# Optimization experiments

Measured on AMD Instinct MI355X. Metric: run time of the kernel, lower is better.

## Reference

```python
import jax, jax.numpy as jnp
import numpy as np

EPS = 1e-5
NUM_HEADS = 4


def _layer_norm(x, g, b):
    m = jnp.mean(x, axis=-1, keepdims=True)
    v = jnp.mean((x - m) ** 2, axis=-1, keepdims=True)
    return (x - m) / jnp.sqrt(v + EPS) * g + b


def setup_inputs() -> dict:
    key = jax.random.key(0)
    ks = jax.random.split(key, 32)
    B, N, ND, TD, L = 100000, 20, 128, 64, 2
    HD = 128  # num_heads * attention_dim
    CD = ND + TD  # 192
    s = 0.02
    inp = {
        "node_features": jax.random.normal(ks[0], (B, ND), jnp.float32),
        "neighbor_features": jax.random.normal(ks[1], (B, N, ND), jnp.float32),
        "node_times": jax.random.uniform(ks[2], (B,), jnp.float32),
        "neighbor_times": jax.random.uniform(ks[3], (B, N), jnp.float32),
        "time_freq": jax.random.normal(ks[4], (TD,), jnp.float32),
        "time_phase": jnp.zeros((TD,), jnp.float32),
        "Wq": jax.random.normal(ks[5], (L, CD, HD), jnp.float32) * s,
        "bq": jnp.zeros((L, HD), jnp.float32),
        "Wk": jax.random.normal(ks[6], (L, CD, HD), jnp.float32) * s,
        "bk": jnp.zeros((L, HD), jnp.float32),
        "Wv": jax.random.normal(ks[7], (L, CD, HD), jnp.float32) * s,
        "bv": jnp.zeros((L, HD), jnp.float32),
        "Wo": jax.random.normal(ks[8], (L, HD, ND), jnp.float32) * s,
        "bo": jnp.zeros((L, ND), jnp.float32),
        "W1": jax.random.normal(ks[9], (L, ND, 2 * ND), jnp.float32) * s,
        "b1": jnp.zeros((L, 2 * ND), jnp.float32),
        "W2": jax.random.normal(ks[10], (L, 2 * ND, ND), jnp.float32) * s,
        "b2": jnp.zeros((L, ND), jnp.float32),
        "g1": jnp.ones((L, ND), jnp.float32),
        "be1": jnp.zeros((L, ND), jnp.float32),
        "g2": jnp.ones((L, ND), jnp.float32),
        "be2": jnp.zeros((L, ND), jnp.float32),
        "Wc1": jax.random.normal(ks[11], (ND, ND // 2), jnp.float32) * s,
        "bc1": jnp.zeros((ND // 2,), jnp.float32),
        "Wc2": jax.random.normal(ks[12], (ND // 2, 1), jnp.float32) * s,
        "bc2": jnp.zeros((1,), jnp.float32),
        "mask": jax.random.randint(ks[13], (B, N), 0, 2, jnp.int32),
    }
    return inp


def reference(node_features, neighbor_features, node_times, neighbor_times,
              time_freq, time_phase, Wq, bq, Wk, bk, Wv, bv, Wo, bo,
              W1, b1, W2, b2, g1, be1, g2, be2, Wc1, bc1, Wc2, bc2, mask):
    L, _, HD = Wq.shape
    B, N, ND = neighbor_features.shape
    H = NUM_HEADS
    D = HD // H
    scale = 1.0 / np.sqrt(D).astype(np.float32)
    # time encodings (Bochner): cos(t * w + phi)
    tq = jnp.cos(node_times[:, None] * time_freq + time_phase)          # [B, TD]
    tk = jnp.cos(neighbor_times[..., None] * time_freq + time_phase)   # [B, N, TD]
    kcomb = jnp.concatenate([neighbor_features, tk], axis=-1)           # [B, N, CD]
    pad = (mask == 0)[:, None, :]                                       # [B, 1, N]
    x = node_features
    for l in range(L):
        qcomb = jnp.concatenate([x, tq], axis=-1)                       # [B, CD]
        q = (qcomb @ Wq[l] + bq[l]).reshape(B, H, D)
        k = (kcomb @ Wk[l] + bk[l]).reshape(B, N, H, D)
        v = (kcomb @ Wv[l] + bv[l]).reshape(B, N, H, D)
        scores = jnp.einsum('bhd,bnhd->bhn', q, k) * scale              # [B, H, N]
        scores = jnp.where(pad, jnp.float32(-1e9), scores)
        w = jax.nn.softmax(scores, axis=-1)
        a = jnp.einsum('bhn,bnhd->bhd', w, v).reshape(B, HD)
        attn = a @ Wo[l] + bo[l]                                        # [B, ND]
        x = _layer_norm(x + attn, g1[l], be1[l])
        ff = jax.nn.relu(x @ W1[l] + b1[l]) @ W2[l] + b2[l]
        x = _layer_norm(x + ff, g2[l], be2[l])
    h = jax.nn.relu(x @ Wc1 + bc1)
    return jax.nn.sigmoid(h @ Wc2 + bc2)                                # [B, 1]
```

## Files before the change

kernel.cpp:

```cpp
#include <hip/hip_runtime.h>

#define BB 100000
#define NN 20
#define ND 128
#define TD 64
#define CD 192
#define HD 128
#define NH 4
#define DH 32
#define NL 2

typedef __attribute__((ext_vector_type(8))) short bf16x8;
typedef __attribute__((ext_vector_type(4))) float f32x4;

static __device__ __forceinline__ float bf2f(unsigned short u) {
  return __uint_as_float(((unsigned)u) << 16);
}
static __device__ __forceinline__ unsigned short f2bf(float x) {
  unsigned b = __float_as_uint(x);
  return (unsigned short)((b + 0x7FFFu + ((b >> 16) & 1u)) >> 16);
}
static __device__ __forceinline__ bf16x8 load_a8(const float* p) {
  float4 a = *(const float4*)p, b = *(const float4*)(p + 4);
  bf16x8 r;
  r[0] = (short)f2bf(a.x); r[1] = (short)f2bf(a.y);
  r[2] = (short)f2bf(a.z); r[3] = (short)f2bf(a.w);
  r[4] = (short)f2bf(b.x); r[5] = (short)f2bf(b.y);
  r[6] = (short)f2bf(b.z); r[7] = (short)f2bf(b.w);
  return r;
}


__global__ __launch_bounds__(256) void conv_w(
    const float* __restrict__ Wq, const float* __restrict__ Wk,
    const float* __restrict__ Wv, const float* __restrict__ Wo,
    const float* __restrict__ W1, const float* __restrict__ W2,
    unsigned short* __restrict__ WF) {
  int t = blockIdx.x;
  int l = t / 304, tt = t % 304;
#pragma unroll
  for (int e = 0; e < 2; ++e) {
    int idx = threadIdx.x * 2 + e;
    int lane = idx >> 3, j = idx & 7;
    int wk = ((lane >> 4) << 3) + j;
    int c16 = lane & 15;
    float v;
    if (tt < 48) {
      int kt = tt >> 3, n2 = tt & 7;
      v = Wq[((size_t)l * CD + kt * 32 + wk) * HD + n2 * 16 + c16];
    } else if (tt < 96) {
      int t2 = tt - 48; int h = t2 / 12, n2 = t2 % 12;
      v = Wk[((size_t)l * CD + n2 * 16 + c16) * HD + h * 32 + wk];
    } else if (tt < 144) {
      int t2 = tt - 96; int h = t2 / 12, r2 = t2 % 12, kt = r2 >> 1, n2 = r2 & 1;
      v = Wv[((size_t)l * CD + kt * 32 + wk) * HD + h * 32 + n2 * 16 + c16];
    } else if (tt < 176) {
      int t2 = tt - 144; int kt = t2 >> 3, n2 = t2 & 7;
      v = Wo[((size_t)l * HD + kt * 32 + wk) * ND + n2 * 16 + c16];
    } else if (tt < 240) {
      int t2 = tt - 176; int kt = t2 >> 4, n2 = t2 & 15;
      v = W1[((size_t)l * ND + kt * 32 + wk) * (2 * ND) + n2 * 16 + c16];
    } else {
      int t2 = tt - 240; int kt = t2 >> 3, n2 = t2 & 7;
      v = W2[((size_t)l * 2 * ND + kt * 32 + wk) * ND + n2 * 16 + c16];
    }
    WF[(size_t)l * 155648 + (size_t)tt * 512 + idx] = f2bf(v);
  }
}

__global__ __launch_bounds__(256) void prep_tq(
    const float* __restrict__ ntime, const float* __restrict__ tf,
    const float* __restrict__ tp, float* __restrict__ tqf) {
  int i = blockIdx.x * 256 + threadIdx.x;
  int b = i >> 6, j = i & 63;
  tqf[i] = __cosf(ntime[b] * tf[j] + tp[j]);
}

__global__ __launch_bounds__(256) void prep_mb(const int* __restrict__ mask,
                                               unsigned* __restrict__ mb) {
  int e = blockIdx.x * 256 + threadIdx.x;
  if (e < BB) {
    unsigned m = 0;
    for (int n = 0; n < NN; ++n)
      m |= (mask[(size_t)e * NN + n] != 0 ? 1u : 0u) << n;
    mb[e] = m;
  }
}

template <int TN, int ABF, int OBF>
__global__ __launch_bounds__(256) void gemm16(
    const void* __restrict__ A, int lda,
    const float* __restrict__ A2, int lda2, int ksplit,
    const unsigned short* __restrict__ BF,
    int ktiles, int ntiles, int aKoffMul, int cColMul, int segBMul,
    const float* __restrict__ bias,
    void* __restrict__ C, int ldc, int relu) {
  const int tid = threadIdx.x;
  const int wv = tid >> 6, lane = tid & 63;
  const int NW = blockDim.x >> 6;
  const int m0 = blockIdx.x << 4;
  const int seg = blockIdx.y;
  const int arow = m0 + (lane & 15);
  const int kgrp = (lane >> 4) << 3;
  const int aK = seg * aKoffMul;
  const unsigned short* Bseg = BF + (size_t)seg * segBMul * 512;
  f32x4 acc[TN];
#pragma unroll
  for (int i = 0; i < TN; ++i) acc[i] = f32x4{0.f, 0.f, 0.f, 0.f};
  for (int kt = 0; kt < ktiles; ++kt) {
    bf16x8 af;
    if (kt * 32 >= ksplit) {
      af = load_a8(A2 + (size_t)arow * lda2 + (kt * 32 - ksplit) + kgrp);
    } else if (ABF) {
      af = *(const bf16x8*)((const unsigned short*)A + (size_t)arow * lda + aK +
                            kt * 32 + kgrp);
    } else {
      af = load_a8((const float*)A + (size_t)arow * lda + aK + kt * 32 + kgrp);
    }
#pragma unroll
    for (int i = 0; i < TN; ++i) {
      int nt = wv + NW * i;
      bf16x8 bf = *(const bf16x8*)(Bseg + (((size_t)(kt * ntiles + nt)) << 9) +
                                   (lane << 3));
      acc[i] = __builtin_amdgcn_mfma_f32_16x16x32_bf16(af, bf, acc[i], 0, 0, 0);
    }
  }
  const int crow = m0 + ((lane >> 4) << 2);
#pragma unroll
  for (int i = 0; i < TN; ++i) {
    int nt = wv + NW * i;
    int col = seg * cColMul + nt * 16 + (lane & 15);
    float bv = bias ? bias[col] : 0.f;
#pragma unroll
    for (int rr = 0; rr < 4; ++rr) {
      float v = acc[i][rr] + bv;
      if (relu) v = fmaxf(v, 0.f);
      if (OBF)
        ((unsigned short*)C)[(size_t)(crow + rr) * ldc + col] = f2bf(v);
      else
        ((float*)C)[(size_t)(crow + rr) * ldc + col] = v;
    }
  }
}

template <int ABF, int CLS>
__global__ __launch_bounds__(256) void gemm_ln(
    const void* __restrict__ A, int lda, int ktiles,
    const unsigned short* __restrict__ BF,
    const float* __restrict__ bias, const float* __restrict__ res,
    const float* __restrict__ gamma, const float* __restrict__ beta,
    float* __restrict__ xout,
    const float* __restrict__ Wc1, const float* __restrict__ bc1,
    const float* __restrict__ Wc2, const float* __restrict__ bc2,
    float* __restrict__ out) {
  __shared__ float Cs[16][132];
  __shared__ float hsh[CLS ? 16 : 1][64];
  const int tid = threadIdx.x;
  const int wv = tid >> 6, lane = tid & 63;
  const int m0 = blockIdx.x << 4;
  const int arow = m0 + (lane & 15);
  const int kgrp = (lane >> 4) << 3;
  const int nt0 = wv, nt1 = wv + 4;
  f32x4 acc0 = {0.f, 0.f, 0.f, 0.f}, acc1 = {0.f, 0.f, 0.f, 0.f};
  for (int kt = 0; kt < ktiles; ++kt) {
    bf16x8 af;
    if (ABF)
      af = *(const bf16x8*)((const unsigned short*)A + (size_t)arow * lda +
                            kt * 32 + kgrp);
    else
      af = load_a8((const float*)A + (size_t)arow * lda + kt * 32 + kgrp);
    bf16x8 b0 = *(const bf16x8*)(BF + (((size_t)(kt * 8 + nt0)) << 9) + (lane << 3));
    bf16x8 b1 = *(const bf16x8*)(BF + (((size_t)(kt * 8 + nt1)) << 9) + (lane << 3));
    acc0 = __builtin_amdgcn_mfma_f32_16x16x32_bf16(af, b0, acc0, 0, 0, 0);
    acc1 = __builtin_amdgcn_mfma_f32_16x16x32_bf16(af, b1, acc1, 0, 0, 0);
  }
  {
    const int lrow = (lane >> 4) << 2;
    int c0 = nt0 * 16 + (lane & 15), c1 = nt1 * 16 + (lane & 15);
    float bv0 = bias[c0], bv1 = bias[c1];
#pragma unroll
    for (int rr = 0; rr < 4; ++rr) {
      Cs[lrow + rr][c0] = acc0[rr] + bv0;
      Cs[lrow + rr][c1] = acc1[rr] + bv1;
    }
  }
  __syncthreads();
#pragma unroll
  for (int rr = 0; rr < 4; ++rr) {
    int rw = wv * 4 + rr;
    size_t grow = (size_t)(m0 + rw) * ND;
    float y0 = Cs[rw][lane] + res[grow + lane];
    float y1 = Cs[rw][lane + 64] + res[grow + lane + 64];
    float s = y0 + y1, ss = y0 * y0 + y1 * y1;
#pragma unroll
    for (int off = 32; off > 0; off >>= 1) {
      s += __shfl_xor(s, off);
      ss += __shfl_xor(ss, off);
    }
    float mean = s * (1.f / ND);
    float var = ss * (1.f / ND) - mean * mean;
    float rstd = rsqrtf(var + 1e-5f);
    float x0 = (y0 - mean) * rstd * gamma[lane] + beta[lane];
    float x1 = (y1 - mean) * rstd * gamma[lane + 64] + beta[lane + 64];
    if (CLS) {
      Cs[rw][lane] = x0;
      Cs[rw][lane + 64] = x1;
    } else {
      xout[grow + lane] = x0;
      xout[grow + lane + 64] = x1;
    }
  }
  if (CLS) {
    __syncthreads();
#pragma unroll
    for (int rep = 0; rep < 4; ++rep) {
      int idx = rep * 256 + tid;
      int row = idx >> 6, j = idx & 63;
      float a = 0.f;
      for (int c = 0; c < ND; ++c) a += Cs[row][c] * Wc1[c * 64 + j];
      hsh[row][j] = fmaxf(a + bc1[j], 0.f);
    }
    __syncthreads();
#pragma unroll
    for (int rr = 0; rr < 4; ++rr) {
      int row = wv * 4 + rr;
      float p = hsh[row][lane] * Wc2[lane];
#pragma unroll
      for (int off = 32; off > 0; off >>= 1) p += __shfl_xor(p, off);
      if (lane == 0)
        out[m0 + row] = 1.f / (1.f + expf(-(p + bc2[0])));
    }
  }
}

__global__ __launch_bounds__(256) void attn_b(
    const float* __restrict__ nbf, const float* __restrict__ nbt,
    const float* __restrict__ tf, const float* __restrict__ tp,
    const unsigned* __restrict__ mb, const unsigned short* __restrict__ r,
    unsigned short* __restrict__ u) {
  __shared__ __align__(16) unsigned short kcb[2][NN][200];
  __shared__ __align__(16) float rs[2][768];
  __shared__ __align__(16) float scs[2][NH][NN];
  __shared__ unsigned msks[2];
  const int tid = threadIdx.x;
  const size_t e0 = (size_t)blockIdx.x * 2;

  if (tid < 192) {
    uint4 v = *(const uint4*)(r + e0 * 768 + tid * 8);
    const unsigned short* pv = (const unsigned short*)&v;
    float* dst = &rs[0][0] + tid * 8;
#pragma unroll
    for (int k = 0; k < 8; ++k) dst[k] = bf2f(pv[k]);
  }
  for (int i = tid; i < 2 * NN * 32; i += 256) {
    int el = i / (NN * 32), rem = i % (NN * 32);
    int n = rem >> 5, cq = rem & 31;
    float4 v = *(const float4*)&nbf[((e0 + el) * NN + n) * ND + cq * 4];
    ushort4 o;
    o.x = f2bf(v.x); o.y = f2bf(v.y); o.z = f2bf(v.z); o.w = f2bf(v.w);
    *(ushort4*)&kcb[el][n][cq * 4] = o;
  }
  for (int i = tid; i < 2 * NN * 32; i += 256) {
    int el = i / (NN * 32), rem = i % (NN * 32);
    int n = rem >> 5, jp = (rem & 31) * 2;
    float t = nbt[(e0 + el) * NN + n];
    unsigned a = f2bf(__cosf(t * tf[jp] + tp[jp]));
    unsigned b = f2bf(__cosf(t * tf[jp + 1] + tp[jp + 1]));
    *(unsigned*)&kcb[el][n][ND + jp] = a | (b << 16);
  }
  if (tid < 2) msks[tid] = mb[e0 + tid];
  __syncthreads();
  if (tid < 2 * NH * NN) {
    int el = tid / (NH * NN), rem = tid % (NH * NN);
    int h = rem / NN, n = rem % NN;
    const float* rp = &rs[el][h * CD];
    const unsigned short* kp = &kcb[el][n][0];
    float acc = 0.f;
    for (int c = 0; c < CD; c += 4) {
      float4 rv = *(const float4*)&rp[c];
      ushort4 kv = *(const ushort4*)&kp[c];
      acc += rv.x * bf2f(kv.x) + rv.y * bf2f(kv.y) + rv.z * bf2f(kv.z) +
             rv.w * bf2f(kv.w);
    }
    scs[el][h][n] =
        ((msks[el] >> n) & 1u) ? acc * 0.17677669529663687f : -1e9f;
  }
  __syncthreads();
  if (tid < 2 * NH) {
    int el = tid >> 2, h = tid & 3;
    float mx = -3.4e38f;
#pragma unroll
    for (int n = 0; n < NN; ++n) mx = fmaxf(mx, scs[el][h][n]);
    float ev[NN], s = 0.f;
#pragma unroll
    for (int n = 0; n < NN; ++n) { ev[n] = __expf(scs[el][h][n] - mx); s += ev[n]; }
    float inv = 1.f / s;
#pragma unroll
    for (int n = 0; n < NN; ++n) scs[el][h][n] = ev[n] * inv;
  }
  __syncthreads();
  for (int i = tid; i < 2 * NH * (CD / 4); i += 256) {
    int el = i / (NH * 48), rem = i % (NH * 48);
    int h = rem / 48, cq = (rem % 48) * 4;
    float a0 = 0.f, a1 = 0.f, a2 = 0.f, a3 = 0.f;
#pragma unroll
    for (int n = 0; n < NN; ++n) {
      float w = scs[el][h][n];
      ushort4 kv = *(const ushort4*)&kcb[el][n][cq];
      a0 += w * bf2f(kv.x); a1 += w * bf2f(kv.y);
      a2 += w * bf2f(kv.z); a3 += w * bf2f(kv.w);
    }
    ushort4 o;
    o.x = f2bf(a0); o.y = f2bf(a1); o.z = f2bf(a2); o.w = f2bf(a3);
    *(ushort4*)&u[(e0 + el) * 768 + h * CD + cq] = o;
  }
}

#define G 2
#define T 256
#define KCS 196
#define RUS 772

__global__ __launch_bounds__(T, 4) void tgat_fused(
    const float* __restrict__ nf, const float* __restrict__ nbf,
    const float* __restrict__ nt, const float* __restrict__ nbt,
    const float* __restrict__ tf, const float* __restrict__ tp,
    const float* __restrict__ Wq, const float* __restrict__ bq,
    const float* __restrict__ Wk,
    const float* __restrict__ Wv, const float* __restrict__ bv,
    const float* __restrict__ Wo, const float* __restrict__ bo,
    const float* __restrict__ W1, const float* __restrict__ b1,
    const float* __restrict__ W2, const float* __restrict__ b2,
    const float* __restrict__ g1, const float* __restrict__ be1,
    const float* __restrict__ g2, const float* __restrict__ be2,
    const float* __restrict__ Wc1, const float* __restrict__ bc1,
    const float* __restrict__ Wc2, const float* __restrict__ bc2,
    const int* __restrict__ mask,
    float* __restrict__ out) {
  __shared__ __align__(16) unsigned short kc[G][NN][KCS];
  __shared__ __align__(16) float xs[G][ND];
  __shared__ __align__(16) float tqs[G][TD];
  __shared__ __align__(16) float ys[G][HD];
  __shared__ __align__(16) float rus[G][RUS];
  __shared__ __align__(16) float scs[G][NH][NN];
  __shared__ __align__(16) float h1s[G][2 * ND];
  __shared__ __align__(16) unsigned msks[G];
  float* asv = &h1s[0][0];
  const int tid = threadIdx.x;
  const int b0 = blockIdx.x * G;
  {
    int g = tid >> 7, j = tid & 127;
    xs[g][j] = nf[(b0 + g) * ND + j];
  }
  if (tid < G * TD) {
    int g = tid >> 6, j = tid & 63;
    tqs[g][j] = __cosf(nt[b0 + g] * tf[j] + tp[j]);
  }
  if (tid < G) {
    unsigned m = 0;
    for (int n = 0; n < NN; ++n)
      m |= (mask[(b0 + tid) * NN + n] != 0 ? 1u : 0u) << n;
    msks[tid] = m;
  }
  for (int idx = tid; idx < G * NN * (ND / 4); idx += T) {
    int g = idx / (NN * 32), rem = idx % (NN * 32);
    int n = rem >> 5, cq = rem & 31;
    float4 v = *(const float4*)&nbf[(((b0 + g) * NN + n) * ND) + cq * 4];
    ushort4 o;
    o.x = f2bf(v.x); o.y = f2bf(v.y); o.z = f2bf(v.z); o.w = f2bf(v.w);
    *(ushort4*)&kc[g][n][cq * 4] = o;
  }
  for (int idx = tid; idx < G * NN * TD; idx += T) {
    int g = idx / (NN * TD), rem = idx % (NN * TD);
    int n = rem >> 6, j = rem & 63;
    kc[g][n][ND + j] = f2bf(__cosf(nbt[(b0 + g) * NN + n] * tf[j] + tp[j]));
  }
  __syncthreads();
  const float scale = 0.17677669529663687f;
  for (int l = 0; l < NL; ++l) {
    {
      int g = tid >> 7, j = tid & 127;
      const float* wq = Wq + (l * CD) * HD + j;
      float acc = bq[l * HD + j];
      for (int c = 0; c < CD; c += 4) {
        float4 qv = (c < ND) ? *(const float4*)&xs[g][c]
                             : *(const float4*)&tqs[g][c - ND];
        acc += qv.x * wq[(c + 0) * HD] + qv.y * wq[(c + 1) * HD] +
               qv.z * wq[(c + 2) * HD] + qv.w * wq[(c + 3) * HD];
      }
      ys[g][j] = acc;
    }
    __syncthreads();
    for (int rep = 0; rep < 3; ++rep) {
      int i = rep * T + tid;
      int h = i / CD;
      int c2 = i - h * CD;
      const float* wk = Wk + (l * CD + c2) * HD + h * DH;
      const float* yp0 = &ys[0][h * DH];
      const float* yp1 = &ys[1][h * DH];
      float a0 = 0.f, a1 = 0.f;
#pragma unroll
      for (int d = 0; d < DH; d += 4) {
        float4 w4 = *(const float4*)&wk[d];
        float4 y0 = *(const float4*)&yp0[d];
        float4 y1 = *(const float4*)&yp1[d];
        a0 += y0.x * w4.x + y0.y * w4.y + y0.z * w4.z + y0.w * w4.w;
        a1 += y1.x * w4.x + y1.y * w4.y + y1.z * w4.z + y1.w * w4.w;
      }
      rus[0][i] = a0;
      rus[1][i] = a1;
    }
    __syncthreads();
    if (tid < G * NH * NN) {
      int g = tid / (NH * NN), rem = tid % (NH * NN);
      int h = rem / NN, n = rem % NN;
      const float* rp = &rus[g][h * CD];
      const unsigned short* kp = &kc[g][n][0];
      float acc = 0.f;
      for (int c = 0; c < CD; c += 4) {
        float4 rv = *(const float4*)&rp[c];
        ushort4 kv = *(const ushort4*)&kp[c];
        acc += rv.x * bf2f(kv.x) + rv.y * bf2f(kv.y) + rv.z * bf2f(kv.z) +
               rv.w * bf2f(kv.w);
      }
      scs[g][h][n] = ((msks[g] >> n) & 1u) ? acc * scale : -1e9f;
    }
    __syncthreads();
    if (tid < G * NH) {
      int g = tid / NH, h = tid % NH;
      float mx = -3.4e38f;
#pragma unroll
      for (int n = 0; n < NN; ++n) mx = fmaxf(mx, scs[g][h][n]);
      float ev[NN], s = 0.f;
#pragma unroll
      for (int n = 0; n < NN; ++n) { ev[n] = __expf(scs[g][h][n] - mx); s += ev[n]; }
      float inv = 1.f / s;
#pragma unroll
      for (int n = 0; n < NN; ++n) scs[g][h][n] = ev[n] * inv;
    }
    __syncthreads();
    for (int flat = tid; flat < G * NH * (CD / 4); flat += T) {
      int g = flat / (NH * 48), iq = flat % (NH * 48);
      int h = iq / 48, c = (iq % 48) * 4;
      const unsigned short* kp = &kc[g][0][0];
      float a0 = 0.f, a1 = 0.f, a2 = 0.f, a3 = 0.f;
#pragma unroll
      for (int n = 0; n < NN; ++n) {
        float w = scs[g][h][n];
        ushort4 kv = *(const ushort4*)&kp[n * KCS + c];
        a0 += w * bf2f(kv.x); a1 += w * bf2f(kv.y);
        a2 += w * bf2f(kv.z); a3 += w * bf2f(kv.w);
      }
      *(float4*)&rus[g][h * CD + c] = make_float4(a0, a1, a2, a3);
    }
    __syncthreads();
    {
      int j = tid & (HD - 1);
      int g = tid >> 7;
      int h = j >> 5;
      const float* wv = Wv + (l * CD) * HD + j;
      float acc = 0.f;
      for (int c = 0; c < CD; c += 4) {
        float4 uv = *(const float4*)&rus[g][h * CD + c];
        acc += uv.x * wv[(c + 0) * HD] + uv.y * wv[(c + 1) * HD] +
               uv.z * wv[(c + 2) * HD] + uv.w * wv[(c + 3) * HD];
      }
      asv[g * HD + j] = acc + bv[l * HD + j];
    }
    __syncthreads();
    {
      int j = tid & (ND - 1);
      int g = tid >> 7;
      const float* wo = Wo + (l * HD) * ND + j;
      float acc = 0.f;
      for (int c = 0; c < HD; c += 4) {
        float4 av = *(const float4*)&asv[g * HD + c];
        acc += av.x * wo[(c + 0) * ND] + av.y * wo[(c + 1) * ND] +
               av.z * wo[(c + 2) * ND] + av.w * wo[(c + 3) * ND];
      }
      rus[g][j] = acc + bo[l * ND + j];
    }
    __syncthreads();
    if (tid < G * 64) {
      int g = tid >> 6, lane = tid & 63;
      float y0 = xs[g][lane] + rus[g][lane];
      float y1 = xs[g][lane + 64] + rus[g][lane + 64];
      float s = y0 + y1, ss = y0 * y0 + y1 * y1;
#pragma unroll
      for (int off = 32; off > 0; off >>= 1) {
        s += __shfl_xor(s, off);
        ss += __shfl_xor(ss, off);
      }
      float mean = s * (1.f / ND);
      float var = ss * (1.f / ND) - mean * mean;
      float rstd = rsqrtf(var + 1e-5f);
      xs[g][lane] = (y0 - mean) * rstd * g1[l * ND + lane] + be1[l * ND + lane];
      xs[g][lane + 64] =
          (y1 - mean) * rstd * g1[l * ND + lane + 64] + be1[l * ND + lane + 64];
    }
    __syncthreads();
    {
      int j = tid;
      const float* w1p = W1 + (l * ND) * (2 * ND) + j;
      float acc0 = 0.f, acc1 = 0.f;
      for (int c = 0; c < ND; c += 4) {
        float w0 = w1p[(c + 0) * 2 * ND], wa = w1p[(c + 1) * 2 * ND],
              w2 = w1p[(c + 2) * 2 * ND], w3 = w1p[(c + 3) * 2 * ND];
        float4 x0 = *(const float4*)&xs[0][c];
        float4 x1 = *(const float4*)&xs[1][c];
        acc0 += x0.x * w0 + x0.y * wa + x0.z * w2 + x0.w * w3;
        acc1 += x1.x * w0 + x1.y * wa + x1.z * w2 + x1.w * w3;
      }
      float b1v = b1[l * 2 * ND + j];
      h1s[0][j] = fmaxf(acc0 + b1v, 0.f);
      h1s[1][j] = fmaxf(acc1 + b1v, 0.f);
    }
    __syncthreads();
    {
      int j = tid & (ND - 1);
      int g = tid >> 7;
      const float* w2p = W2 + (l * 2 * ND) * ND + j;
      float acc = 0.f;
      for (int c = 0; c < 2 * ND; c += 4) {
        float4 hv = *(const float4*)&h1s[g][c];
        acc += hv.x * w2p[(c + 0) * ND] + hv.y * w2p[(c + 1) * ND] +
               hv.z * w2p[(c + 2) * ND] + hv.w * w2p[(c + 3) * ND];
      }
      rus[g][j] = acc + b2[l * ND + j];
    }
    __syncthreads();
    if (tid < G * 64) {
      int g = tid >> 6, lane = tid & 63;
      float y0 = xs[g][lane] + rus[g][lane];
      float y1 = xs[g][lane + 64] + rus[g][lane + 64];
      float s = y0 + y1, ss = y0 * y0 + y1 * y1;
#pragma unroll
      for (int off = 32; off > 0; off >>= 1) {
        s += __shfl_xor(s, off);
        ss += __shfl_xor(ss, off);
      }
      float mean = s * (1.f / ND);
      float var = ss * (1.f / ND) - mean * mean;
      float rstd = rsqrtf(var + 1e-5f);
      xs[g][lane] = (y0 - mean) * rstd * g2[l * ND + lane] + be2[l * ND + lane];
      xs[g][lane + 64] =
          (y1 - mean) * rstd * g2[l * ND + lane + 64] + be2[l * ND + lane + 64];
    }
    __syncthreads();
  }
  if (tid < G * 64) {
    int j = tid & 63;
    int g = tid >> 6;
    const float* wc = Wc1 + j;
    float acc = 0.f;
    for (int c = 0; c < ND; c += 4) {
      float4 xv = *(const float4*)&xs[g][c];
      acc += xv.x * wc[(c + 0) * 64] + xv.y * wc[(c + 1) * 64] +
             xv.z * wc[(c + 2) * 64] + xv.w * wc[(c + 3) * 64];
    }
    ((float*)scs)[g * 64 + j] = fmaxf(acc + bc1[j], 0.f);
  }
  __syncthreads();
  if (tid < G * 64) {
    int g = tid >> 6, lane = tid & 63;
    float p = ((float*)scs)[g * 64 + lane] * Wc2[lane];
#pragma unroll
    for (int off = 32; off > 0; off >>= 1) p += __shfl_xor(p, off);
    if (lane == 0) {
      float z = p + bc2[0];
      out[b0 + g] = 1.f / (1.f + expf(-z));
    }
  }
}

extern "C" void kernel_launch(void* const* d_in, const int* in_sizes, int n_in,
                              void* d_out, int out_size, void* d_ws,
                              size_t ws_size, hipStream_t stream) {
  (void)in_sizes; (void)n_in; (void)out_size;
  const float* nf  = (const float*)d_in[0];
  const float* nbf = (const float*)d_in[1];
  const float* ntm = (const float*)d_in[2];
  const float* nbt = (const float*)d_in[3];
  const float* tf  = (const float*)d_in[4];
  const float* tp  = (const float*)d_in[5];
  const float* Wq  = (const float*)d_in[6];
  const float* bq  = (const float*)d_in[7];
  const float* Wk  = (const float*)d_in[8];
  const float* Wv  = (const float*)d_in[10];
  const float* bv  = (const float*)d_in[11];
  const float* Wo  = (const float*)d_in[12];
  const float* bo  = (const float*)d_in[13];
  const float* W1  = (const float*)d_in[14];
  const float* b1  = (const float*)d_in[15];
  const float* W2  = (const float*)d_in[16];
  const float* b2  = (const float*)d_in[17];
  const float* g1  = (const float*)d_in[18];
  const float* be1 = (const float*)d_in[19];
  const float* g2  = (const float*)d_in[20];
  const float* be2 = (const float*)d_in[21];
  const float* Wc1 = (const float*)d_in[22];
  const float* bc1 = (const float*)d_in[23];
  const float* Wc2 = (const float*)d_in[24];
  const float* bc2 = (const float*)d_in[25];
  const int* mask  = (const int*)d_in[26];
  float* out = (float*)d_out;

  const size_t NEED = 333822592ull;
  if (ws_size >= NEED) {
    char* w = (char*)d_ws;
    unsigned short* WF = (unsigned short*)w;
    unsigned* mb = (unsigned*)(w + 622592);
    float* tqf = (float*)(w + 1022592);
    unsigned short* yb = (unsigned short*)(w + 26622592);
    unsigned short* rb = (unsigned short*)(w + 52222592);
    unsigned short* ab = (unsigned short*)(w + 205822592);
    unsigned short* h1b = (unsigned short*)(w + 231422592);
    float* xfb = (float*)(w + 282622592);

    conv_w<<<608, 256, 0, stream>>>(Wq, Wk, Wv, Wo, W1, W2, WF);
    prep_tq<<<25000, 256, 0, stream>>>(ntm, tf, tp, tqf);
    prep_mb<<<(BB + 255) / 256, 256, 0, stream>>>(mask, mb);

    const float* xsrc = nf;
    for (int l = 0; l < NL; ++l) {
      const unsigned short* WFl = WF + (size_t)l * 155648;
      gemm16<2, 0, 1><<<dim3(6250, 1), 256, 0, stream>>>(
          xsrc, ND, tqf, TD, 128, WFl, 6, 8, 0, 0, 0, bq + l * HD, yb, HD, 0);
      gemm16<3, 1, 1><<<dim3(6250, 4), 256, 0, stream>>>(
          yb, HD, nullptr, 0, 1 << 30, WFl + 24576, 1, 12, DH, 192, 12,
          nullptr, rb, 768, 0);
      attn_b<<<50000, 256, 0, stream>>>(nbf, nbt, tf, tp, mb, rb, rb);
      gemm16<1, 1, 1><<<dim3(6250, 4), 128, 0, stream>>>(
          rb, 768, nullptr, 0, 1 << 30, WFl + 49152, 6, 2, 192, DH, 12,
          bv + l * HD, ab, HD, 0);
      gemm_ln<1, 0><<<6250, 256, 0, stream>>>(
          ab, HD, 4, WFl + 73728, bo + l * ND, xsrc, g1 + l * ND,
          be1 + l * ND, xfb, nullptr, nullptr, nullptr, nullptr, nullptr);
      gemm16<4, 0, 1><<<dim3(6250, 1), 256, 0, stream>>>(
          xfb, ND, nullptr, 0, 1 << 30, WFl + 90112, 4, 16, 0, 0, 0,
          b1 + l * 2 * ND, h1b, 2 * ND, 1);
      if (l == NL - 1)
        gemm_ln<1, 1><<<6250, 256, 0, stream>>>(
            h1b, 2 * ND, 8, WFl + 122880, b2 + l * ND, xfb, g2 + l * ND,
            be2 + l * ND, xfb, Wc1, bc1, Wc2, bc2, out);
      else
        gemm_ln<1, 0><<<6250, 256, 0, stream>>>(
            h1b, 2 * ND, 8, WFl + 122880, b2 + l * ND, xfb, g2 + l * ND,
            be2 + l * ND, xfb, nullptr, nullptr, nullptr, nullptr, nullptr);
      xsrc = xfb;
    }
  } else {
    tgat_fused<<<BB / G, T, 0, stream>>>(nf, nbf, ntm, nbt, tf, tp, Wq, bq, Wk,
                                         Wv, bv, Wo, bo, W1, b1, W2, b2, g1,
                                         be1, g2, be2, Wc1, bc1, Wc2, bc2,
                                         mask, out);
  }
}
```

Baseline: 1.405 ms.

## Fuse Q-projection with key-folding GEMM and fuse attn-out, LN1, FF1 into one kernel

Merges the query projection and the per-head Wk-folding GEMM into one kernel that keeps the intermediate query tile in shared memory instead of a global bf16 buffer. It also fuses the V-projection GEMM, the output projection with bias, residual and LayerNorm, and the first FFN GEMM with ReLU into a single per-16-row kernel, staging intermediates in LDS. This drops several kernel launches and the global round trips for yb, ab and the xfb re-read, and shrinks the workspace. The trade-off is larger LDS use, more syncthreads, and less parallelism per launch, since the 4-way segment grid dimension is gone.

```diff
diff --git a/kernel.cpp b/kernel.cpp
--- a/kernel.cpp
+++ b/kernel.cpp
@@ -87,58 +87,169 @@
   }
 }
 
-template <int TN, int ABF, int OBF>
-__global__ __launch_bounds__(256) void gemm16(
-    const void* __restrict__ A, int lda,
-    const float* __restrict__ A2, int lda2, int ksplit,
-    const unsigned short* __restrict__ BF,
-    int ktiles, int ntiles, int aKoffMul, int cColMul, int segBMul,
-    const float* __restrict__ bias,
-    void* __restrict__ C, int ldc, int relu) {
+__global__ __launch_bounds__(256) void gemm_yr(
+    const float* __restrict__ A, const float* __restrict__ tqf,
+    const unsigned short* __restrict__ WFl, const float* __restrict__ bq,
+    unsigned short* __restrict__ rb) {
+  __shared__ unsigned short ylds[16][136];
   const int tid = threadIdx.x;
   const int wv = tid >> 6, lane = tid & 63;
-  const int NW = blockDim.x >> 6;
   const int m0 = blockIdx.x << 4;
-  const int seg = blockIdx.y;
   const int arow = m0 + (lane & 15);
   const int kgrp = (lane >> 4) << 3;
-  const int aK = seg * aKoffMul;
-  const unsigned short* Bseg = BF + (size_t)seg * segBMul * 512;
-  f32x4 acc[TN];
-#pragma unroll
-  for (int i = 0; i < TN; ++i) acc[i] = f32x4{0.f, 0.f, 0.f, 0.f};
-  for (int kt = 0; kt < ktiles; ++kt) {
-    bf16x8 af;
-    if (kt * 32 >= ksplit) {
-      af = load_a8(A2 + (size_t)arow * lda2 + (kt * 32 - ksplit) + kgrp);
-    } else if (ABF) {
-      af = *(const bf16x8*)((const unsigned short*)A + (size_t)arow * lda + aK +
-                            kt * 32 + kgrp);
-    } else {
-      af = load_a8((const float*)A + (size_t)arow * lda + aK + kt * 32 + kgrp);
-    }
-#pragma unroll
-    for (int i = 0; i < TN; ++i) {
-      int nt = wv + NW * i;
-      bf16x8 bf = *(const bf16x8*)(Bseg + (((size_t)(kt * ntiles + nt)) << 9) +
-                                   (lane << 3));
+  {
+    f32x4 acc[2];
+    acc[0] = f32x4{0.f, 0.f, 0.f, 0.f};
+    acc[1] = f32x4{0.f, 0.f, 0.f, 0.f};
+    for (int kt = 0; kt < 6; ++kt) {
+      bf16x8 af = (kt < 4)
+                      ? load_a8(A + (size_t)arow * ND + kt * 32 + kgrp)
+                      : load_a8(tqf + (size_t)arow * TD + (kt - 4) * 32 + kgrp);
+#pragma unroll
+      for (int i = 0; i < 2; ++i) {
+        int nt = wv + 4 * i;
+        bf16x8 bf = *(const bf16x8*)(WFl + (((size_t)(kt * 8 + nt)) << 9) +
+                                     (lane << 3));
+        acc[i] = __builtin_amdgcn_mfma_f32_16x16x32_bf16(af, bf, acc[i], 0, 0, 0);
+      }
+    }
+    int lrow = (lane >> 4) << 2;
+#pragma unroll
+    for (int i = 0; i < 2; ++i) {
+      int col = (wv + 4 * i) * 16 + (lane & 15);
+      float bv = bq[col];
+#pragma unroll
+      for (int rr = 0; rr < 4; ++rr)
+        ylds[lrow + rr][col] = f2bf(acc[i][rr] + bv);
+    }
+  }
+  __syncthreads();
+  {
+    f32x4 acc[12];
+#pragma unroll
+    for (int i = 0; i < 12; ++i) acc[i] = f32x4{0.f, 0.f, 0.f, 0.f};
+    bf16x8 af = *(const bf16x8*)&ylds[lane & 15][wv * 32 + kgrp];
+    const unsigned short* B = WFl + 24576 + (size_t)wv * 12 * 512;
+#pragma unroll
+    for (int i = 0; i < 12; ++i) {
+      bf16x8 bf = *(const bf16x8*)(B + (((size_t)i) << 9) + (lane << 3));
       acc[i] = __builtin_amdgcn_mfma_f32_16x16x32_bf16(af, bf, acc[i], 0, 0, 0);
     }
-  }
-  const int crow = m0 + ((lane >> 4) << 2);
-#pragma unroll
-  for (int i = 0; i < TN; ++i) {
-    int nt = wv + NW * i;
-    int col = seg * cColMul + nt * 16 + (lane & 15);
-    float bv = bias ? bias[col] : 0.f;
+    int crow = m0 + ((lane >> 4) << 2);
+#pragma unroll
+    for (int i = 0; i < 12; ++i) {
+      int col = wv * 192 + i * 16 + (lane & 15);
+#pragma unroll
+      for (int rr = 0; rr < 4; ++rr)
+        rb[(size_t)(crow + rr) * 768 + col] = f2bf(acc[i][rr]);
+    }
+  }
+}
+
+__global__ __launch_bounds__(256) void gemm_aln1ff1(
+    const unsigned short* __restrict__ u, const unsigned short* __restrict__ WFl,
+    const float* __restrict__ bv, const float* __restrict__ bo,
+    const float* __restrict__ res, const float* __restrict__ gamma,
+    const float* __restrict__ beta, const float* __restrict__ b1,
+    float* __restrict__ xout, unsigned short* __restrict__ h1b) {
+  __shared__ unsigned short alds[16][136];
+  __shared__ float Cs[16][132];
+  const int tid = threadIdx.x;
+  const int wv = tid >> 6, lane = tid & 63;
+  const int m0 = blockIdx.x << 4;
+  const int arow = m0 + (lane & 15);
+  const int kgrp = (lane >> 4) << 3;
+  {
+    f32x4 acc0 = {0.f, 0.f, 0.f, 0.f}, acc1 = {0.f, 0.f, 0.f, 0.f};
+    const unsigned short* B = WFl + 49152 + (size_t)wv * 12 * 512;
+    for (int kt = 0; kt < 6; ++kt) {
+      bf16x8 af = *(const bf16x8*)(u + (size_t)arow * 768 + wv * 192 +
+                                   kt * 32 + kgrp);
+      bf16x8 b0 = *(const bf16x8*)(B + (((size_t)(kt * 2 + 0)) << 9) + (lane << 3));
+      bf16x8 b1f = *(const bf16x8*)(B + (((size_t)(kt * 2 + 1)) << 9) + (lane << 3));
+      acc0 = __builtin_amdgcn_mfma_f32_16x16x32_bf16(af, b0, acc0, 0, 0, 0);
+      acc1 = __builtin_amdgcn_mfma_f32_16x16x32_bf16(af, b1f, acc1, 0, 0, 0);
+    }
+    int lrow = (lane >> 4) << 2;
+    int c0 = wv * 32 + (lane & 15), c1 = wv * 32 + 16 + (lane & 15);
+    float bv0 = bv[c0], bv1 = bv[c1];
 #pragma unroll
     for (int rr = 0; rr < 4; ++rr) {
-      float v = acc[i][rr] + bv;
-      if (relu) v = fmaxf(v, 0.f);
-      if (OBF)
-        ((unsigned short*)C)[(size_t)(crow + rr) * ldc + col] = f2bf(v);
-      else
-        ((float*)C)[(size_t)(crow + rr) * ldc + col] = v;
+      alds[lrow + rr][c0] = f2bf(acc0[rr] + bv0);
+      alds[lrow + rr][c1] = f2bf(acc1[rr] + bv1);
+    }
+  }
+  __syncthreads();
+  {
+    const int nt0 = wv, nt1 = wv + 4;
+    f32x4 acc0 = {0.f, 0.f, 0.f, 0.f}, acc1 = {0.f, 0.f, 0.f, 0.f};
+    for (int kt = 0; kt < 4; ++kt) {
+      bf16x8 af = *(const bf16x8*)&alds[lane & 15][kt * 32 + kgrp];
+      bf16x8 b0 = *(const bf16x8*)(WFl + 73728 +
+                                   (((size_t)(kt * 8 + nt0)) << 9) + (lane << 3));
+      bf16x8 b1f = *(const bf16x8*)(WFl + 73728 +
+                                    (((size_t)(kt * 8 + nt1)) << 9) + (lane << 3));
+      acc0 = __builtin_amdgcn_mfma_f32_16x16x32_bf16(af, b0, acc0, 0, 0, 0);
+      acc1 = __builtin_amdgcn_mfma_f32_16x16x32_bf16(af, b1f, acc1, 0, 0, 0);
+    }
+    {
+      int lrow = (lane >> 4) << 2;
+      int c0 = nt0 * 16 + (lane & 15), c1 = nt1 * 16 + (lane & 15);
+      float bv0 = bo[c0], bv1 = bo[c1];
+#pragma unroll
+      for (int rr = 0; rr < 4; ++rr) {
+        Cs[lrow + rr][c0] = acc0[rr] + bv0;
+        Cs[lrow + rr][c1] = acc1[rr] + bv1;
+      }
+    }
+    __syncthreads();
+#pragma unroll
+    for (int rr = 0; rr < 4; ++rr) {
+      int rw = wv * 4 + rr;
+      size_t grow = (size_t)(m0 + rw) * ND;
+      float y0 = Cs[rw][lane] + res[grow + lane];
+      float y1 = Cs[rw][lane + 64] + res[grow + lane + 64];
+      float s = y0 + y1, ss = y0 * y0 + y1 * y1;
+#pragma unroll
+      for (int off = 32; off > 0; off >>= 1) {
+        s += __shfl_xor(s, off);
+        ss += __shfl_xor(ss, off);
+      }
+      float mean = s * (1.f / ND);
+      float var = ss * (1.f / ND) - mean * mean;
+      float rstd = rsqrtf(var + 1e-5f);
+      float x0 = (y0 - mean) * rstd * gamma[lane] + beta[lane];
+      float x1 = (y1 - mean) * rstd * gamma[lane + 64] + beta[lane + 64];
+      xout[grow + lane] = x0;
+      xout[grow + lane + 64] = x1;
+      Cs[rw][lane] = x0;
+      Cs[rw][lane + 64] = x1;
+    }
+  }
+  __syncthreads();
+  {
+    f32x4 acc[4];
+#pragma unroll
+    for (int i = 0; i < 4; ++i) acc[i] = f32x4{0.f, 0.f, 0.f, 0.f};
+    for (int kt = 0; kt < 4; ++kt) {
+      bf16x8 af = load_a8(&Cs[lane & 15][kt * 32 + kgrp]);
+#pragma unroll
+      for (int i = 0; i < 4; ++i) {
+        int nt = wv + 4 * i;
+        bf16x8 bf = *(const bf16x8*)(WFl + 90112 +
+                                     (((size_t)(kt * 16 + nt)) << 9) + (lane << 3));
+        acc[i] = __builtin_amdgcn_mfma_f32_16x16x32_bf16(af, bf, acc[i], 0, 0, 0);
+      }
+    }
+    int crow = m0 + ((lane >> 4) << 2);
+#pragma unroll
+    for (int i = 0; i < 4; ++i) {
+      int col = (wv + 4 * i) * 16 + (lane & 15);
+      float bvv = b1[col];
+#pragma unroll
+      for (int rr = 0; rr < 4; ++rr)
+        h1b[(size_t)(crow + rr) * (2 * ND) + col] =
+            f2bf(fmaxf(acc[i][rr] + bvv, 0.f));
     }
   }
 }
@@ -605,17 +716,15 @@
   const int* mask  = (const int*)d_in[26];
   float* out = (float*)d_out;
 
-  const size_t NEED = 333822592ull;
+  const size_t NEED = 282622592ull;
   if (ws_size >= NEED) {
     char* w = (char*)d_ws;
     unsigned short* WF = (unsigned short*)w;
     unsigned* mb = (unsigned*)(w + 622592);
     float* tqf = (float*)(w + 1022592);
-    unsigned short* yb = (unsigned short*)(w + 26622592);
-    unsigned short* rb = (unsigned short*)(w + 52222592);
-    unsigned short* ab = (unsigned short*)(w + 205822592);
-    unsigned short* h1b = (unsigned short*)(w + 231422592);
-    float* xfb = (float*)(w + 282622592);
+    unsigned short* rb = (unsigned short*)(w + 26622592);
+    unsigned short* h1b = (unsigned short*)(w + 180222592);
+    float* xfb = (float*)(w + 231422592);
 
     conv_w<<<608, 256, 0, stream>>>(Wq, Wk, Wv, Wo, W1, W2, WF);
     prep_tq<<<25000, 256, 0, stream>>>(ntm, tf, tp, tqf);
@@ -624,21 +733,11 @@
     const float* xsrc = nf;
     for (int l = 0; l < NL; ++l) {
       const unsigned short* WFl = WF + (size_t)l * 155648;
-      gemm16<2, 0, 1><<<dim3(6250, 1), 256, 0, stream>>>(
-          xsrc, ND, tqf, TD, 128, WFl, 6, 8, 0, 0, 0, bq + l * HD, yb, HD, 0);
-      gemm16<3, 1, 1><<<dim3(6250, 4), 256, 0, stream>>>(
-          yb, HD, nullptr, 0, 1 << 30, WFl + 24576, 1, 12, DH, 192, 12,
-          nullptr, rb, 768, 0);
+      gemm_yr<<<6250, 256, 0, stream>>>(xsrc, tqf, WFl, bq + l * HD, rb);
       attn_b<<<50000, 256, 0, stream>>>(nbf, nbt, tf, tp, mb, rb, rb);
-      gemm16<1, 1, 1><<<dim3(6250, 4), 128, 0, stream>>>(
-          rb, 768, nullptr, 0, 1 << 30, WFl + 49152, 6, 2, 192, DH, 12,
-          bv + l * HD, ab, HD, 0);
-      gemm_ln<1, 0><<<6250, 256, 0, stream>>>(
-          ab, HD, 4, WFl + 73728, bo + l * ND, xsrc, g1 + l * ND,
-          be1 + l * ND, xfb, nullptr, nullptr, nullptr, nullptr, nullptr);
-      gemm16<4, 0, 1><<<dim3(6250, 1), 256, 0, stream>>>(
-          xfb, ND, nullptr, 0, 1 << 30, WFl + 90112, 4, 16, 0, 0, 0,
-          b1 + l * 2 * ND, h1b, 2 * ND, 1);
+      gemm_aln1ff1<<<6250, 256, 0, stream>>>(
+          rb, WFl, bv + l * HD, bo + l * ND, xsrc, g1 + l * ND, be1 + l * ND,
+          b1 + l * 2 * ND, xfb, h1b);
       if (l == NL - 1)
         gemm_ln<1, 1><<<6250, 256, 0, stream>>>(
             h1b, 2 * ND, 8, WFl + 122880, b2 + l * ND, xfb, g2 + l * ND,
```

After: 1.288 ms, median of 2. 1.09x faster.
